# Performance work log

Measured on AMD Instinct MI355X. Metric: run time of the kernel, lower is better.

The kernel has to match this reference:

```python
import jax, jax.numpy as jnp
import numpy as np

P = 50000    # number of POIs (rows of HG_pu, size of square A)
U = 100000   # number of users (rows of HG_up)
NNZ = 1600000
D = 128      # emb_dim


def setup_inputs() -> dict:
    key = jax.random.key(0)
    ks = jax.random.split(key, 8)
    x = jax.random.normal(ks[0], (P, D), dtype=jnp.float32)
    e = jax.random.normal(ks[1], (P, D), dtype=jnp.float32)
    vals_up = jax.random.uniform(ks[2], (NNZ,), dtype=jnp.float32)
    vals_pu = jax.random.uniform(ks[3], (NNZ,), dtype=jnp.float32)
    rows_up = jax.random.randint(ks[4], (NNZ,), 0, U, dtype=jnp.int32)
    cols_up = jax.random.randint(ks[5], (NNZ,), 0, P, dtype=jnp.int32)
    rows_pu = jax.random.randint(ks[6], (NNZ,), 0, P, dtype=jnp.int32)
    cols_pu = jax.random.randint(ks[7], (NNZ,), 0, U, dtype=jnp.int32)
    return {"t": 0, "x": x, "e": e,
            "vals_up": vals_up, "vals_pu": vals_pu,
            "rows_up": rows_up, "cols_up": cols_up,
            "rows_pu": rows_pu, "cols_pu": cols_pu}


def _spmm(vals, rows, cols, dense, num_rows):
    # sparse [num_rows, *] @ dense -> [num_rows, D]
    gathered = vals[:, None] * dense[cols]          # [nnz, D]
    return jax.ops.segment_sum(gathered, rows, num_segments=num_rows)


def reference(t, x, e, vals_up, vals_pu, rows_up, cols_up, rows_pu, cols_pu):
    # A = HG_pu @ HG_up (never materialized);  out = (A - I) @ x + e
    y = _spmm(vals_up, rows_up, cols_up, x, U)      # HG_up @ x : [U, D]
    z = _spmm(vals_pu, rows_pu, cols_pu, y, P)      # HG_pu @ y : [P, D]
    return z - x + e                                # (A - I) x + e
```

## Files before the change

kernel.cpp:

```cpp
#include <hip/hip_runtime.h>

#define NP 50000
#define NU 100000
#define NNZ_C 1600000
#define NNZ2 (2 * NNZ_C)
#define DIM 128
#define NR_TOT (NU + NP)

#define RBSH 7
#define RB 128
#define NBK ((NR_TOT + RB - 1) / RB)
#define ITEMS 4096
#define NBLK ((NNZ2 + ITEMS - 1) / ITEMS)
#define CHUNK 4096
#define CPT (CHUNK / 256)
#define CVT_NW (NP * 64)
#define CVT_BLKS ((CVT_NW + 255) / 256)

#define CAP_UP 2600
#define CAP_PU 4900
#define NSLOT (1172 * CAP_UP + 391 * (CAP_PU - CAP_UP))
__device__ __host__ inline int bkt_base(int b) {
    return b * CAP_UP + (b > 781 ? (b - 781) * (CAP_PU - CAP_UP) : 0);
}

__device__ inline unsigned pack_bf16x2(float a, float b) {
    unsigned ia = __float_as_uint(a), ib = __float_as_uint(b);
    ia = (ia + 0x7FFFu + ((ia >> 16) & 1u)) >> 16;
    ib = (ib + 0x7FFFu + ((ib >> 16) & 1u)) >> 16;
    return ia | (ib << 16);
}

__device__ inline float dec_val(unsigned p) {
    return __uint_as_float((p & 0x7FFFu) << 16);
}

__global__ void cvt_bf16_kernel(const float* __restrict__ x,
                                unsigned* __restrict__ xh,
                                int* __restrict__ gcur) {
    if (blockIdx.x == 0) {
        for (int k = threadIdx.x; k < NBK; k += 256) gcur[k] = 0;
    }
    int i = blockIdx.x * 256 + threadIdx.x;
    if (i < CVT_NW) {
        float2 v = ((const float2*)x)[i];
        xh[i] = pack_bf16x2(v.x, v.y);
    }
}

__global__ void p1_scatter_kernel(const float* __restrict__ vals_up,
                                  const float* __restrict__ vals_pu,
                                  const int* __restrict__ rows_up,
                                  const int* __restrict__ rows_pu,
                                  const int* __restrict__ cols_up,
                                  const int* __restrict__ cols_pu,
                                  int* __restrict__ gcur,
                                  unsigned* __restrict__ stag_pay,
                                  unsigned char* __restrict__ stag_row) {
    __shared__ unsigned spay[CHUNK];
    __shared__ unsigned sdr[CHUNK];
    __shared__ int h[NBK];
    __shared__ int cb[NBK];
    __shared__ int ws[4];

    int tid = threadIdx.x;
    int blk = blockIdx.x;
    for (int k = tid; k < NBK; k += 256) h[k] = 0;
    __syncthreads();

    int cbeg = blk * ITEMS;
    int cnt_items = NNZ2 - cbeg;
    if (cnt_items > CHUNK) cnt_items = CHUNK;

    unsigned rpay[CPT];
    int rrow[CPT];
    for (int k = 0; k < CPT; ++k) {
        int i = cbeg + k * 256 + tid;
        if (i < NNZ2) {
            int r, cc; float v;
            if (i < NNZ_C) { r = rows_up[i]; cc = cols_up[i]; v = vals_up[i]; }
            else { int q = i - NNZ_C; r = NU + rows_pu[q]; cc = cols_pu[q]; v = vals_pu[q]; }
            unsigned vb = __float_as_uint(v);
            unsigned vr = (vb + 0x7FFFu + ((vb >> 16) & 1u)) >> 16;
            rpay[k] = ((unsigned)cc << 15) | vr;
            rrow[k] = r;
            atomicAdd(&h[r >> RBSH], 1);
        } else {
            rrow[k] = -1;
        }
    }
    __syncthreads();

    {
        int s0 = tid * 5;
        int s1 = s0 + 5; if (s1 > NBK) s1 = NBK; if (s0 > NBK) s0 = NBK;
        int a = 0;
        for (int s = s0; s < s1; ++s) {
            int c = h[s];
            a += c;
            cb[s] = bkt_base(s) + (c ? atomicAdd(&gcur[s], c) : 0);
        }
        int lane = tid & 63, wid = tid >> 6;
        int v = a;
        for (int d = 1; d < 64; d <<= 1) {
            int t = __shfl_up(v, d);
            if (lane >= d) v += t;
        }
        if (lane == 63) ws[wid] = v;
        __syncthreads();
        int woff = 0;
        for (int w = 0; w < wid; ++w) woff += ws[w];
        int run = woff + v - a;
        for (int s = s0; s < s1; ++s) { int c = h[s]; h[s] = run; run += c; }
    }
    __syncthreads();

    for (int k = 0; k < CPT; ++k) {
        if (rrow[k] < 0) continue;
        int b = rrow[k] >> RBSH;
        int slot = atomicAdd(&h[b], 1);
        int d = atomicAdd(&cb[b], 1);
        spay[slot] = rpay[k];
        sdr[slot] = ((unsigned)d << 7) | (unsigned)(rrow[k] & (RB - 1));
    }
    __syncthreads();

    for (int s = tid; s < cnt_items; s += 256) {
        unsigned q = sdr[s];
        int d = (int)(q >> 7);
        stag_pay[d] = spay[s];
        stag_row[d] = (unsigned char)(q & 127u);
    }
}

__global__ void p2_finalize_kernel(const unsigned* __restrict__ stag_pay,
                                   const unsigned char* __restrict__ stag_row,
                                   const int* __restrict__ gcur,
                                   unsigned* __restrict__ packed,
                                   int* __restrict__ row_beg,
                                   int* __restrict__ row_cnt) {
    __shared__ int cnt[RB];
    __shared__ int cur[RB];
    __shared__ int wtot;
    int b = blockIdx.x;
    int tid = threadIdx.x;
    int beg = bkt_base(b), end = beg + gcur[b];
    if (tid < RB) cnt[tid] = 0;
    __syncthreads();
    for (int i = beg + tid; i < end; i += 256)
        atomicAdd(&cnt[stag_row[i]], 1);
    __syncthreads();
    if (tid < RB) {
        int a = cnt[tid];
        int lane = tid & 63;
        int v = a;
        for (int d = 1; d < 64; d <<= 1) {
            int t = __shfl_up(v, d);
            if (lane >= d) v += t;
        }
        if (tid == 63) wtot = v;
        __syncthreads();
        if (tid >= 64) v += wtot;
        int excl = v - a;
        cur[tid] = beg + excl;
        int rr = (b << RBSH) + tid;
        if (rr < NR_TOT) { row_beg[rr] = beg + excl; row_cnt[rr] = a; }
    } else {
        __syncthreads();
    }
    __syncthreads();
    for (int i = beg + tid; i < end; i += 256) {
        int pos = atomicAdd(&cur[stag_row[i]], 1);
        packed[pos] = stag_pay[i];
    }
}


#define NZ_FMA(P, U)                                            \
    do {                                                         \
        acc.x += dec_val(P) * __uint_as_float((U) << 16);        \
        acc.y += dec_val(P) * __uint_as_float((U) & 0xFFFF0000u);\
    } while (0)

__device__ inline void gather_row(const unsigned* __restrict__ packed,
                                  const unsigned* __restrict__ src,
                                  int beg, int end, int lane, float2& acc) {
    beg = __builtin_amdgcn_readfirstlane(beg);
    end = __builtin_amdgcn_readfirstlane(end);
    int n = end - beg;
    const unsigned* prow = packed + beg;
    int j = 0;
    for (; j + 8 <= n; j += 8) {
        unsigned p0 = prow[j + 0];
        unsigned p1 = prow[j + 1];
        unsigned p2 = prow[j + 2];
        unsigned p3 = prow[j + 3];
        unsigned p4 = prow[j + 4];
        unsigned p5 = prow[j + 5];
        unsigned p6 = prow[j + 6];
        unsigned p7 = prow[j + 7];
        unsigned u0 = src[(p0 >> 15) * 64 + lane];
        unsigned u1 = src[(p1 >> 15) * 64 + lane];
        unsigned u2 = src[(p2 >> 15) * 64 + lane];
        unsigned u3 = src[(p3 >> 15) * 64 + lane];
        unsigned u4 = src[(p4 >> 15) * 64 + lane];
        unsigned u5 = src[(p5 >> 15) * 64 + lane];
        unsigned u6 = src[(p6 >> 15) * 64 + lane];
        unsigned u7 = src[(p7 >> 15) * 64 + lane];
        NZ_FMA(p0, u0); NZ_FMA(p1, u1); NZ_FMA(p2, u2); NZ_FMA(p3, u3);
        NZ_FMA(p4, u4); NZ_FMA(p5, u5); NZ_FMA(p6, u6); NZ_FMA(p7, u7);
    }
    for (; j + 4 <= n; j += 4) {
        unsigned p0 = prow[j + 0];
        unsigned p1 = prow[j + 1];
        unsigned p2 = prow[j + 2];
        unsigned p3 = prow[j + 3];
        unsigned u0 = src[(p0 >> 15) * 64 + lane];
        unsigned u1 = src[(p1 >> 15) * 64 + lane];
        unsigned u2 = src[(p2 >> 15) * 64 + lane];
        unsigned u3 = src[(p3 >> 15) * 64 + lane];
        NZ_FMA(p0, u0); NZ_FMA(p1, u1); NZ_FMA(p2, u2); NZ_FMA(p3, u3);
    }
    for (; j < n; ++j) {
        unsigned p = prow[j];
        unsigned u = src[(p >> 15) * 64 + lane];
        NZ_FMA(p, u);
    }
}

__global__ void spmm_gather_kernel(const int* __restrict__ row_beg,
                                   const int* __restrict__ row_cnt,
                                   const unsigned* __restrict__ packed,
                                   const unsigned* __restrict__ src,
                                   unsigned* __restrict__ dst) {
    int r = blockIdx.x * 4 + (threadIdx.x >> 6);
    if (r >= NU) return;
    int lane = threadIdx.x & 63;
    int beg = row_beg[r], end = beg + row_cnt[r];
    float2 acc = make_float2(0.f, 0.f);
    gather_row(packed, src, beg, end, lane, acc);
    dst[r * 64 + lane] = pack_bf16x2(acc.x, acc.y);
}

__global__ void spmm_gather_fused_kernel(const int* __restrict__ row_beg,
                                         const int* __restrict__ row_cnt,
                                         const unsigned* __restrict__ packed,
                                         const unsigned* __restrict__ src,
                                         const float* __restrict__ x,
                                         const float* __restrict__ e,
                                         float* __restrict__ out) {
    int r = blockIdx.x * 4 + (threadIdx.x >> 6);
    if (r >= NP) return;
    int lane = threadIdx.x & 63;
    int beg = row_beg[NU + r], end = beg + row_cnt[NU + r];
    float2 acc = make_float2(0.f, 0.f);
    gather_row(packed, src, beg, end, lane, acc);
    float2 xv = ((const float2*)(x + (size_t)r * DIM))[lane];
    float2 ev = ((const float2*)(e + (size_t)r * DIM))[lane];
    float2 o;
    o.x = acc.x - xv.x + ev.x;
    o.y = acc.y - xv.y + ev.y;
    ((float2*)(out + (size_t)r * DIM))[lane] = o;
}

extern "C" void kernel_launch(void* const* d_in, const int* in_sizes, int n_in,
                              void* d_out, int out_size, void* d_ws, size_t ws_size,
                              hipStream_t stream) {
    const float* x       = (const float*)d_in[1];
    const float* e       = (const float*)d_in[2];
    const float* vals_up = (const float*)d_in[3];
    const float* vals_pu = (const float*)d_in[4];
    const int*   rows_up = (const int*)d_in[5];
    const int*   cols_up = (const int*)d_in[6];
    const int*   rows_pu = (const int*)d_in[7];
    const int*   cols_pu = (const int*)d_in[8];
    float* out = (float*)d_out;

    char* ws = (char*)d_ws;
    unsigned* yh          = (unsigned*)(ws);
    unsigned* stag_pay    = (unsigned*)(ws);
    unsigned char* stag_row = (unsigned char*)(ws + 16000000);
    unsigned* xh     = (unsigned*)(ws + 25600000);
    unsigned* packed = (unsigned*)(ws + 38400000);
    int* gcur        = (int*)(ws + 54866496);
    int* row_beg     = (int*)(ws + 54875904);
    int* row_cnt     = (int*)(ws + 55475904);

    cvt_bf16_kernel<<<CVT_BLKS, 256, 0, stream>>>(x, xh, gcur);

    p1_scatter_kernel<<<NBLK, 256, 0, stream>>>(vals_up, vals_pu,
                                                rows_up, rows_pu,
                                                cols_up, cols_pu,
                                                gcur, stag_pay, stag_row);
    p2_finalize_kernel<<<NBK, 256, 0, stream>>>(stag_pay, stag_row, gcur,
                                                packed, row_beg, row_cnt);

    spmm_gather_kernel<<<(NU + 3) / 4, 256, 0, stream>>>(row_beg, row_cnt,
                                                         packed, xh, yh);

    spmm_gather_fused_kernel<<<(NP + 3) / 4, 256, 0, stream>>>(row_beg, row_cnt,
                                                               packed, yh,
                                                               x, e, out);
}
```

Baseline: 356.4 us.

## Replace bucketed two-pass CSR build with per-row histogram, scan, and atomic scatter

The old build staged entries into fixed-capacity 128-row buckets with shared-memory sorting, then ran a second finalize pass. The new version counts nonzeros per row with global atomics (fused with the x-to-bf16 conversion) and turns the counts into row offsets with a three-kernel scan. It then scatters each entry directly to its final slot with a global atomic per row cursor, and the final cursor serves as the row end. This removes the staging buffers and one full read/write pass, but adds global atomic contention, extra small kernel launches, and a nondeterministic order of entries within each row.

```diff
diff --git a/kernel.cpp b/kernel.cpp
--- a/kernel.cpp
+++ b/kernel.cpp
@@ -7,22 +7,16 @@
 #define DIM 128
 #define NR_TOT (NU + NP)
 
-#define RBSH 7
-#define RB 128
-#define NBK ((NR_TOT + RB - 1) / RB)
-#define ITEMS 4096
-#define NBLK ((NNZ2 + ITEMS - 1) / ITEMS)
-#define CHUNK 4096
-#define CPT (CHUNK / 256)
+#define NBK ((NR_TOT + 127) / 128)
 #define CVT_NW (NP * 64)
 #define CVT_BLKS ((CVT_NW + 255) / 256)
 
-#define CAP_UP 2600
-#define CAP_PU 4900
-#define NSLOT (1172 * CAP_UP + 391 * (CAP_PU - CAP_UP))
-__device__ __host__ inline int bkt_base(int b) {
-    return b * CAP_UP + (b > 781 ? (b - 781) * (CAP_PU - CAP_UP) : 0);
-}
+#define HIST_ITEMS 8192
+#define HIST_BLKS ((NNZ2 + HIST_ITEMS - 1) / HIST_ITEMS)
+
+#define SC_IPT 8
+#define SC_ITEMS (256 * SC_IPT)
+#define SC_BLKS ((NNZ2 + SC_ITEMS - 1) / SC_ITEMS)
 
 __device__ inline unsigned pack_bf16x2(float a, float b) {
     unsigned ia = __float_as_uint(a), ib = __float_as_uint(b);
@@ -35,143 +29,112 @@
     return __uint_as_float((p & 0x7FFFu) << 16);
 }
 
-__global__ void cvt_bf16_kernel(const float* __restrict__ x,
-                                unsigned* __restrict__ xh,
-                                int* __restrict__ gcur) {
-    if (blockIdx.x == 0) {
-        for (int k = threadIdx.x; k < NBK; k += 256) gcur[k] = 0;
-    }
+__global__ void zero_kernel(int* __restrict__ row_cnt) {
     int i = blockIdx.x * 256 + threadIdx.x;
-    if (i < CVT_NW) {
-        float2 v = ((const float2*)x)[i];
-        xh[i] = pack_bf16x2(v.x, v.y);
-    }
-}
-
-__global__ void p1_scatter_kernel(const float* __restrict__ vals_up,
-                                  const float* __restrict__ vals_pu,
-                                  const int* __restrict__ rows_up,
-                                  const int* __restrict__ rows_pu,
-                                  const int* __restrict__ cols_up,
-                                  const int* __restrict__ cols_pu,
-                                  int* __restrict__ gcur,
-                                  unsigned* __restrict__ stag_pay,
-                                  unsigned char* __restrict__ stag_row) {
-    __shared__ unsigned spay[CHUNK];
-    __shared__ unsigned sdr[CHUNK];
-    __shared__ int h[NBK];
-    __shared__ int cb[NBK];
-    __shared__ int ws[4];
-
+    if (i < NR_TOT) row_cnt[i] = 0;
+}
+
+__global__ void cvt_rowhist_kernel(const float* __restrict__ x,
+                                   unsigned* __restrict__ xh,
+                                   const int* __restrict__ rows_up,
+                                   const int* __restrict__ rows_pu,
+                                   int* __restrict__ row_cnt) {
+    if (blockIdx.x < HIST_BLKS) {
+        int base = blockIdx.x * HIST_ITEMS;
+        for (int k = 0; k < HIST_ITEMS / 256; ++k) {
+            int i = base + k * 256 + threadIdx.x;
+            if (i >= NNZ2) break;
+            int r = (i < NNZ_C) ? rows_up[i] : (NU + rows_pu[i - NNZ_C]);
+            atomicAdd(&row_cnt[r], 1);
+        }
+    } else {
+        int i = (blockIdx.x - HIST_BLKS) * 256 + threadIdx.x;
+        if (i < CVT_NW) {
+            float2 v = ((const float2*)x)[i];
+            xh[i] = pack_bf16x2(v.x, v.y);
+        }
+    }
+}
+
+__global__ void row_bsum_kernel(const int* __restrict__ row_cnt,
+                                int* __restrict__ btot) {
+    int b = blockIdx.x;
+    int t = threadIdx.x;
+    int rr = (b << 7) + t;
+    int v = (rr < NR_TOT) ? row_cnt[rr] : 0;
+    for (int d = 32; d >= 1; d >>= 1) v += __shfl_down(v, d);
+    __shared__ int s1;
+    if (t == 64) s1 = v;
+    __syncthreads();
+    if (t == 0) btot[b] = v + s1;
+}
+
+__global__ void row_base_scan_kernel(const int* __restrict__ btot,
+                                     int* __restrict__ bb) {
+    __shared__ int ws[16];
     int tid = threadIdx.x;
-    int blk = blockIdx.x;
-    for (int k = tid; k < NBK; k += 256) h[k] = 0;
+    int t0 = tid * 2;
+    int e0 = (t0 < NBK) ? btot[t0] : 0;
+    int e1 = (t0 + 1 < NBK) ? btot[t0 + 1] : 0;
+    int a = e0 + e1;
+    int lane = tid & 63, wid = tid >> 6;
+    int v = a;
+    for (int d = 1; d < 64; d <<= 1) {
+        int t = __shfl_up(v, d);
+        if (lane >= d) v += t;
+    }
+    if (lane == 63) ws[wid] = v;
     __syncthreads();
-
-    int cbeg = blk * ITEMS;
-    int cnt_items = NNZ2 - cbeg;
-    if (cnt_items > CHUNK) cnt_items = CHUNK;
-
-    unsigned rpay[CPT];
-    int rrow[CPT];
-    for (int k = 0; k < CPT; ++k) {
-        int i = cbeg + k * 256 + tid;
+    int woff = 0;
+    for (int w = 0; w < wid; ++w) woff += ws[w];
+    int excl = woff + v - a;
+    if (t0 < NBK) bb[t0] = excl;
+    if (t0 + 1 < NBK) bb[t0 + 1] = excl + e0;
+}
+
+__global__ void row_beg_kernel(const int* __restrict__ row_cnt,
+                               const int* __restrict__ bb,
+                               int* __restrict__ row_beg,
+                               int* __restrict__ rowcur) {
+    int b = blockIdx.x;
+    int t = threadIdx.x;
+    int rr = (b << 7) + t;
+    int a = (rr < NR_TOT) ? row_cnt[rr] : 0;
+    int lane = t & 63;
+    int v = a;
+    for (int d = 1; d < 64; d <<= 1) {
+        int s = __shfl_up(v, d);
+        if (lane >= d) v += s;
+    }
+    __shared__ int w0;
+    if (t == 63) w0 = v;
+    __syncthreads();
+    int incl = (t >= 64) ? v + w0 : v;
+    int beg = bb[b] + incl - a;
+    if (rr < NR_TOT) { row_beg[rr] = beg; rowcur[rr] = beg; }
+}
+
+__global__ void scatter_kernel(const float* __restrict__ vals_up,
+                               const float* __restrict__ vals_pu,
+                               const int* __restrict__ rows_up,
+                               const int* __restrict__ rows_pu,
+                               const int* __restrict__ cols_up,
+                               const int* __restrict__ cols_pu,
+                               int* __restrict__ rowcur,
+                               unsigned* __restrict__ packed) {
+    int base = blockIdx.x * SC_ITEMS;
+    #pragma unroll
+    for (int k = 0; k < SC_IPT; ++k) {
+        int i = base + k * 256 + threadIdx.x;
         if (i < NNZ2) {
             int r, cc; float v;
             if (i < NNZ_C) { r = rows_up[i]; cc = cols_up[i]; v = vals_up[i]; }
             else { int q = i - NNZ_C; r = NU + rows_pu[q]; cc = cols_pu[q]; v = vals_pu[q]; }
             unsigned vb = __float_as_uint(v);
             unsigned vr = (vb + 0x7FFFu + ((vb >> 16) & 1u)) >> 16;
-            rpay[k] = ((unsigned)cc << 15) | vr;
-            rrow[k] = r;
-            atomicAdd(&h[r >> RBSH], 1);
-        } else {
-            rrow[k] = -1;
+            int d = atomicAdd(&rowcur[r], 1);
+            packed[d] = ((unsigned)cc << 15) | vr;
         }
-    }
-    __syncthreads();
-
-    {
-        int s0 = tid * 5;
-        int s1 = s0 + 5; if (s1 > NBK) s1 = NBK; if (s0 > NBK) s0 = NBK;
-        int a = 0;
-        for (int s = s0; s < s1; ++s) {
-            int c = h[s];
-            a += c;
-            cb[s] = bkt_base(s) + (c ? atomicAdd(&gcur[s], c) : 0);
-        }
-        int lane = tid & 63, wid = tid >> 6;
-        int v = a;
-        for (int d = 1; d < 64; d <<= 1) {
-            int t = __shfl_up(v, d);
-            if (lane >= d) v += t;
-        }
-        if (lane == 63) ws[wid] = v;
-        __syncthreads();
-        int woff = 0;
-        for (int w = 0; w < wid; ++w) woff += ws[w];
-        int run = woff + v - a;
-        for (int s = s0; s < s1; ++s) { int c = h[s]; h[s] = run; run += c; }
-    }
-    __syncthreads();
-
-    for (int k = 0; k < CPT; ++k) {
-        if (rrow[k] < 0) continue;
-        int b = rrow[k] >> RBSH;
-        int slot = atomicAdd(&h[b], 1);
-        int d = atomicAdd(&cb[b], 1);
-        spay[slot] = rpay[k];
-        sdr[slot] = ((unsigned)d << 7) | (unsigned)(rrow[k] & (RB - 1));
-    }
-    __syncthreads();
-
-    for (int s = tid; s < cnt_items; s += 256) {
-        unsigned q = sdr[s];
-        int d = (int)(q >> 7);
-        stag_pay[d] = spay[s];
-        stag_row[d] = (unsigned char)(q & 127u);
-    }
-}
-
-__global__ void p2_finalize_kernel(const unsigned* __restrict__ stag_pay,
-                                   const unsigned char* __restrict__ stag_row,
-                                   const int* __restrict__ gcur,
-                                   unsigned* __restrict__ packed,
-                                   int* __restrict__ row_beg,
-                                   int* __restrict__ row_cnt) {
-    __shared__ int cnt[RB];
-    __shared__ int cur[RB];
-    __shared__ int wtot;
-    int b = blockIdx.x;
-    int tid = threadIdx.x;
-    int beg = bkt_base(b), end = beg + gcur[b];
-    if (tid < RB) cnt[tid] = 0;
-    __syncthreads();
-    for (int i = beg + tid; i < end; i += 256)
-        atomicAdd(&cnt[stag_row[i]], 1);
-    __syncthreads();
-    if (tid < RB) {
-        int a = cnt[tid];
-        int lane = tid & 63;
-        int v = a;
-        for (int d = 1; d < 64; d <<= 1) {
-            int t = __shfl_up(v, d);
-            if (lane >= d) v += t;
-        }
-        if (tid == 63) wtot = v;
-        __syncthreads();
-        if (tid >= 64) v += wtot;
-        int excl = v - a;
-        cur[tid] = beg + excl;
-        int rr = (b << RBSH) + tid;
-        if (rr < NR_TOT) { row_beg[rr] = beg + excl; row_cnt[rr] = a; }
-    } else {
-        __syncthreads();
-    }
-    __syncthreads();
-    for (int i = beg + tid; i < end; i += 256) {
-        int pos = atomicAdd(&cur[stag_row[i]], 1);
-        packed[pos] = stag_pay[i];
     }
 }
 
@@ -229,21 +192,20 @@
 }
 
 __global__ void spmm_gather_kernel(const int* __restrict__ row_beg,
-                                   const int* __restrict__ row_cnt,
+                                   const int* __restrict__ row_end,
                                    const unsigned* __restrict__ packed,
                                    const unsigned* __restrict__ src,
                                    unsigned* __restrict__ dst) {
     int r = blockIdx.x * 4 + (threadIdx.x >> 6);
     if (r >= NU) return;
     int lane = threadIdx.x & 63;
-    int beg = row_beg[r], end = beg + row_cnt[r];
     float2 acc = make_float2(0.f, 0.f);
-    gather_row(packed, src, beg, end, lane, acc);
+    gather_row(packed, src, row_beg[r], row_end[r], lane, acc);
     dst[r * 64 + lane] = pack_bf16x2(acc.x, acc.y);
 }
 
 __global__ void spmm_gather_fused_kernel(const int* __restrict__ row_beg,
-                                         const int* __restrict__ row_cnt,
+                                         const int* __restrict__ row_end,
                                          const unsigned* __restrict__ packed,
                                          const unsigned* __restrict__ src,
                                          const float* __restrict__ x,
@@ -252,9 +214,8 @@
     int r = blockIdx.x * 4 + (threadIdx.x >> 6);
     if (r >= NP) return;
     int lane = threadIdx.x & 63;
-    int beg = row_beg[NU + r], end = beg + row_cnt[NU + r];
     float2 acc = make_float2(0.f, 0.f);
-    gather_row(packed, src, beg, end, lane, acc);
+    gather_row(packed, src, row_beg[NU + r], row_end[NU + r], lane, acc);
     float2 xv = ((const float2*)(x + (size_t)r * DIM))[lane];
     float2 ev = ((const float2*)(e + (size_t)r * DIM))[lane];
     float2 o;
@@ -277,28 +238,33 @@
     float* out = (float*)d_out;
 
     char* ws = (char*)d_ws;
-    unsigned* yh          = (unsigned*)(ws);
-    unsigned* stag_pay    = (unsigned*)(ws);
-    unsigned char* stag_row = (unsigned char*)(ws + 16000000);
+    unsigned* yh     = (unsigned*)(ws);
     unsigned* xh     = (unsigned*)(ws + 25600000);
     unsigned* packed = (unsigned*)(ws + 38400000);
-    int* gcur        = (int*)(ws + 54866496);
-    int* row_beg     = (int*)(ws + 54875904);
-    int* row_cnt     = (int*)(ws + 55475904);
-
-    cvt_bf16_kernel<<<CVT_BLKS, 256, 0, stream>>>(x, xh, gcur);
-
-    p1_scatter_kernel<<<NBLK, 256, 0, stream>>>(vals_up, vals_pu,
+    int* row_cnt     = (int*)(ws + 51200000);
+    int* row_beg     = (int*)(ws + 51800064);
+    int* rowcur      = (int*)(ws + 52400128);
+    int* btot        = (int*)(ws + 53000192);
+    int* bb          = (int*)(ws + 53004880);
+
+    zero_kernel<<<(NR_TOT + 255) / 256, 256, 0, stream>>>(row_cnt);
+
+    cvt_rowhist_kernel<<<HIST_BLKS + CVT_BLKS, 256, 0, stream>>>(
+        x, xh, rows_up, rows_pu, row_cnt);
+
+    row_bsum_kernel<<<NBK, 128, 0, stream>>>(row_cnt, btot);
+    row_base_scan_kernel<<<1, 1024, 0, stream>>>(btot, bb);
+    row_beg_kernel<<<NBK, 128, 0, stream>>>(row_cnt, bb, row_beg, rowcur);
+
+    scatter_kernel<<<SC_BLKS, 256, 0, stream>>>(vals_up, vals_pu,
                                                 rows_up, rows_pu,
                                                 cols_up, cols_pu,
-                                                gcur, stag_pay, stag_row);
-    p2_finalize_kernel<<<NBK, 256, 0, stream>>>(stag_pay, stag_row, gcur,
-                                                packed, row_beg, row_cnt);
-
-    spmm_gather_kernel<<<(NU + 3) / 4, 256, 0, stream>>>(row_beg, row_cnt,
+                                                rowcur, packed);
+
+    spmm_gather_kernel<<<(NU + 3) / 4, 256, 0, stream>>>(row_beg, rowcur,
                                                          packed, xh, yh);
 
-    spmm_gather_fused_kernel<<<(NP + 3) / 4, 256, 0, stream>>>(row_beg, row_cnt,
+    spmm_gather_fused_kernel<<<(NP + 3) / 4, 256, 0, stream>>>(row_beg, rowcur,
                                                                packed, yh,
                                                                x, e, out);
 }
```

Result: slower. 547.3 us (+53.6%).
